# Optimization experiments

Hardware: AMD Instinct MI355X
Metric: run time of the kernel (lower is better)

Reference implementation:

```python
import jax, jax.numpy as jnp
import numpy as np

N_VOCAB, N_REL, D_EMB, D_HID, N_MOTIF = 200000, 50, 128, 128, 85
N_NODES, N_EDGES, N_CENTER, N_NONMOL = 100000, 600000, 512, 20000


def _l2norm(x):
    # torch F.normalize(p=2, dim=1) with eps=1e-12
    n = jnp.linalg.norm(x, axis=1, keepdims=True)
    return x / jnp.maximum(n, 1e-12)


def _gine(x, src, dst, edge_attr, W, b):
    # GINEConv(eps=0): Linear(x + segment_sum(relu(x[src] + edge_attr), dst))
    m = jax.nn.relu(x[src] + edge_attr)            # [E, H]
    agg = jax.ops.segment_sum(m, dst, num_segments=x.shape[0])  # [N, H]
    return (x + agg) @ W + b


def setup_inputs() -> dict:
    key = jax.random.key(0)
    ks = jax.random.split(key, 20)
    s = lambda k, shape, fan: jax.random.normal(k, shape, jnp.float32) * (1.0 / np.sqrt(fan))
    inp = {
        'node_ids': jax.random.randint(ks[0], (N_NODES,), 0, N_VOCAB),
        'rel_ids': jax.random.randint(ks[1], (N_EDGES,), 0, N_REL),
        'center_mol_idx': jax.random.randint(ks[2], (N_CENTER,), 0, N_NODES),
        'non_molecule_node_ids': jax.random.randint(ks[3], (N_NONMOL,), 0, N_NODES),
        'edge_index': jax.random.randint(ks[4], (2, N_EDGES), 0, N_NODES),
        # learned params (weights stored [in, out], i.e. torch W.T)
        'node_emb_table': jax.random.normal(ks[5], (N_VOCAB, D_EMB), jnp.float32),
        'rel_emb_table': jax.random.normal(ks[6], (N_REL, D_EMB), jnp.float32),
        'lin_W': s(ks[7], (D_EMB, D_HID), D_EMB), 'lin_b': jnp.zeros((D_HID,), jnp.float32),
        'W1': s(ks[8], (D_HID, D_HID), D_HID), 'b1': jnp.zeros((D_HID,), jnp.float32),
        'W2': s(ks[9], (D_HID, D_HID), D_HID), 'b2': jnp.zeros((D_HID,), jnp.float32),
        'edge_W': s(ks[10], (2 * D_HID, N_REL), 2 * D_HID), 'edge_b': jnp.zeros((N_REL,), jnp.float32),
        'motif_W': s(ks[11], (D_HID, N_MOTIF), D_HID), 'motif_b': jnp.zeros((N_MOTIF,), jnp.float32),
        'nodec_W': s(ks[12], (D_HID, 15), D_HID), 'nodec_b': jnp.zeros((15,), jnp.float32),
        'bin_W': s(ks[13], (D_HID, 1), D_HID), 'bin_b': jnp.zeros((1,), jnp.float32),
    }
    return inp


def reference(node_ids, rel_ids, center_mol_idx, non_molecule_node_ids, edge_index,
              node_emb_table, rel_emb_table, lin_W, lin_b, W1, b1, W2, b2,
              edge_W, edge_b, motif_W, motif_b, nodec_W, nodec_b, bin_W, bin_b):
    x = _l2norm(node_emb_table[node_ids])          # [N, D]
    e = _l2norm(rel_emb_table[rel_ids])            # [E, D]
    x = jax.nn.relu(x @ lin_W + lin_b)             # [N, H]
    e = jax.nn.relu(e @ lin_W + lin_b)             # [E, H]
    src, dst = edge_index[0], edge_index[1]
    x = jax.nn.relu(_gine(x, src, dst, e, W1, b1))
    x = _gine(x, src, dst, e, W2, b2)              # [N, H]
    edge_pred_input = jnp.concatenate([x[src], x[dst]], axis=1)   # [E, 2H]
    edge_class = edge_pred_input @ edge_W + edge_b                 # [E, num_rels]
    motif_pred = x[center_mol_idx] @ motif_W + motif_b             # [B, num_motifs]
    node_class = x[non_molecule_node_ids] @ nodec_W + nodec_b      # [M, 15]
    binary_pred = x @ bin_W + bin_b                                # [N, 1]
    return (edge_class, motif_pred, node_class, binary_pred)
```

## Files before the change

### kernel.cpp

```cpp
#include <hip/hip_runtime.h>
#include <hip/hip_bf16.h>
#include <math.h>

typedef __hip_bfloat16 bf16;
typedef __attribute__((ext_vector_type(8))) short short8;
typedef __attribute__((ext_vector_type(4))) float float4v;
typedef __attribute__((ext_vector_type(2))) float float2v;
typedef __attribute__((ext_vector_type(2))) unsigned short ushort2v;
typedef __attribute__((ext_vector_type(4))) unsigned short ushort4v;

#define N_NODES_C 100000
#define N_EDGES_C 600000
#define N_CENTER_C 512
#define N_NONMOL_C 20000
#define N_REL_C 50
#define D_C 128
#define N_MOTIF_C 85

#define EO_EDGE  0L
#define EO_MOTIF 30000000L
#define EO_NODEC 30043520L
#define EO_BIN   30343520L

#define AGG_OFF  0L
#define ET_OFF   51200000L
#define WT0_OFF  51225600L
#define WT1_OFF  51258368L
#define WT2_OFF  51291136L
#define BPQ_OFF  51323904L
#define LB_OFF   51352576L
#define B1_OFF   51353088L
#define B2_OFF   51353600L
#define OFFS_OFF 51354112L
#define BSUM_OFF 51755680L
#define SSRC_OFF 51757248L
#define SREL_OFF 54157248L
#define SDST_OFF 56557248L

#define EPW_C 32

__device__ __forceinline__ float b2f(bf16 v) { return __bfloat162float(v); }
__device__ __forceinline__ float bits2f(unsigned short s) {
    unsigned u = ((unsigned)s) << 16; float f; __builtin_memcpy(&f, &u, 4); return f;
}
__device__ __forceinline__ unsigned short f2bits(float f) {
    bf16 h = __float2bfloat16(f); unsigned short s; __builtin_memcpy(&s, &h, 2); return s;
}
__device__ __forceinline__ float ldf(const void* p, size_t i, int isbf) {
    return isbf ? __bfloat162float(((const bf16*)p)[i]) : ((const float*)p)[i];
}
__device__ __forceinline__ void stout_nt(void* p, size_t i, int isbf, float v) {
    if (isbf) __builtin_nontemporal_store(f2bits(v), (unsigned short*)p + i);
    else      __builtin_nontemporal_store(v, (float*)p + i);
}

__global__ void probe_kernel(const void* __restrict__ table, int* __restrict__ flag) {
    __shared__ int bad[256];
    int t = threadIdx.x;
    const bf16* p = (const bf16*)table;
    int cnt = 0;
    for (int i = 0; i < 64; i++) {
        float v = __bfloat162float(p[t * 64 + i]);
        if (!isfinite(v) || fabsf(v) > 1000.0f) cnt++;
    }
    bad[t] = cnt;
    __syncthreads();
    for (int s = 128; s > 0; s >>= 1) {
        if (t < s) bad[t] += bad[t + s];
        __syncthreads();
    }
    if (t == 0) *flag = (bad[0] == 0) ? 1 : 0;
}

__global__ void prepack_kernel(const int* __restrict__ flag,
                               const void* __restrict__ linW, const void* __restrict__ w1,
                               const void* __restrict__ w2, const void* __restrict__ edgeW,
                               const void* __restrict__ linb, const void* __restrict__ bb1,
                               const void* __restrict__ bb2,
                               unsigned short* __restrict__ WT0, unsigned short* __restrict__ WT1,
                               unsigned short* __restrict__ WT2, unsigned short* __restrict__ BPQ,
                               float* __restrict__ LB, float* __restrict__ B1p, float* __restrict__ B2p) {
    int isbf = *flag;
    int g = blockIdx.x * 256 + threadIdx.x;
    if (g < 3 * 16384) {
        int w = g / 16384, i = g % 16384;
        int n = i >> 7, k = i & 127;
        const void* src = (w == 0) ? linW : (w == 1) ? w1 : w2;
        unsigned short* dst = (w == 0) ? WT0 : (w == 1) ? WT1 : WT2;
        dst[i] = f2bits(ldf(src, (size_t)k * 128 + n, isbf));
    } else if (g < 3 * 16384 + 112 * 128) {
        int i = g - 3 * 16384;
        int j = i >> 7, k = i & 127;
        float v = 0.0f;
        if (j < 50)       v = ldf(edgeW, (size_t)k * 50 + j, isbf);
        else if (j < 100) v = ldf(edgeW, (size_t)(128 + k) * 50 + (j - 50), isbf);
        BPQ[i] = f2bits(v);
    } else if (g < 3 * 16384 + 112 * 128 + 3 * 128) {
        int i = g - (3 * 16384 + 112 * 128);
        int w = i >> 7, n = i & 127;
        const void* src = (w == 0) ? linb : (w == 1) ? bb1 : bb2;
        float* dst = (w == 0) ? LB : (w == 1) ? B1p : B2p;
        dst[n] = ldf(src, n, isbf);
    }
}

__global__ void et_kernel(const int* __restrict__ flag,
                          const void* __restrict__ table,
                          const void* __restrict__ W,
                          const void* __restrict__ bias,
                          float* __restrict__ out) {
    int isbf = *flag;
    int row = blockIdx.x;
    int t = threadIdx.x;
    float v = ldf(table, (size_t)row * D_C + t, isbf);
    __shared__ float sv[D_C];
    __shared__ float red[D_C];
    red[t] = v * v;
    __syncthreads();
    for (int s = 64; s > 0; s >>= 1) {
        if (t < s) red[t] += red[t + s];
        __syncthreads();
    }
    float nrm = fmaxf(sqrtf(red[0]), 1e-12f);
    sv[t] = v / nrm;
    __syncthreads();
    float acc = ldf(bias, t, isbf);
    for (int k = 0; k < D_C; k++) acc = fmaf(sv[k], ldf(W, k * D_C + t, isbf), acc);
    out[(size_t)row * D_C + t] = fmaxf(acc, 0.0f);
}

__global__ void normalize_kernel(const int* __restrict__ flag,
                                 const int* __restrict__ ids,
                                 const void* __restrict__ table,
                                 unsigned short* __restrict__ out) {
    int w = (int)((blockIdx.x * (long)blockDim.x + threadIdx.x) >> 6);
    int lane = threadIdx.x & 63;
    if (w >= N_NODES_C) return;
    int isbf = *flag;
    int id = ids[w];
    float v0, v1;
    if (isbf) {
        const unsigned short* p = (const unsigned short*)table + (size_t)id * D_C + lane * 2;
        ushort2 u = *(const ushort2*)p;
        v0 = bits2f(u.x); v1 = bits2f(u.y);
    } else {
        const float* p = (const float*)table + (size_t)id * D_C + lane * 2;
        float2 f = *(const float2*)p;
        v0 = f.x; v1 = f.y;
    }
    float ss = v0 * v0 + v1 * v1;
#pragma unroll
    for (int o = 32; o > 0; o >>= 1) ss += __shfl_down(ss, o, 64);
    ss = __shfl(ss, 0, 64);
    float inv = 1.0f / fmaxf(sqrtf(ss), 1e-12f);
    ushort2 o2;
    o2.x = f2bits(v0 * inv);
    o2.y = f2bits(v1 * inv);
    *(ushort2*)(out + (size_t)w * D_C + lane * 2) = o2;
}

template <int NOUT, bool RELU, bool ADD_AGG, bool HAS_BIAS>
__global__ __launch_bounds__(256, 2) void gemm_kernel(
        const unsigned short* __restrict__ X,
        const float* __restrict__ AGG,
        const unsigned short* __restrict__ BT,
        const float* __restrict__ bias,
        unsigned short* __restrict__ Y,
        int M) {
    constexpr int NT = (NOUT + 15) / 16;
    __shared__ short Als[128 * 128];
    __shared__ short Bls[NT * 16 * 128];
    int t = threadIdx.x;
    int m0 = blockIdx.x * 128;

#pragma unroll
    for (int p = 0; p < 8; p++) {
        int lin = (p * 256 + t) * 8;
        int row = lin >> 7, col = lin & 127;
        int gr = m0 + row; if (gr >= M) gr = M - 1;
        short8 xv = *(const short8*)(X + (size_t)gr * 128 + col);
        if (ADD_AGG) {
            const float* ap = AGG + (size_t)gr * 128 + col;
            float4v a0 = *(const float4v*)ap;
            float4v a1 = *(const float4v*)(ap + 4);
            short8 r;
#pragma unroll
            for (int i = 0; i < 4; i++) r[i] = (short)f2bits(bits2f((unsigned short)xv[i]) + a0[i]);
#pragma unroll
            for (int i = 0; i < 4; i++) r[4 + i] = (short)f2bits(bits2f((unsigned short)xv[4 + i]) + a1[i]);
            xv = r;
        }
        *(short8*)&Als[lin] = xv;
    }
    constexpr int BELEMS = NT * 16 * 128;
#pragma unroll
    for (int p = 0; p * 2048 < BELEMS; p++) {
        int lin = (p * 256 + t) * 8;
        if (lin < BELEMS) *(short8*)&Bls[lin] = *(const short8*)(BT + lin);
    }
    __syncthreads();

    int wave = t >> 6, lane = t & 63;
    int quad = lane >> 4, lr = lane & 15;
    int wr0 = wave * 32;

    short8 afr[2][4];
#pragma unroll
    for (int mt = 0; mt < 2; mt++)
#pragma unroll
        for (int kk = 0; kk < 4; kk++)
            afr[mt][kk] = *(short8*)&Als[(wr0 + mt * 16 + lr) * 128 + kk * 32 + quad * 8];

#pragma unroll
    for (int nt = 0; nt < NT; nt++) {
        short8 bfr[4];
#pragma unroll
        for (int kk = 0; kk < 4; kk++)
            bfr[kk] = *(short8*)&Bls[(nt * 16 + lr) * 128 + kk * 32 + quad * 8];
        int col = nt * 16 + lr;
        float bs = 0.0f;
        if (HAS_BIAS) bs = bias[col];
#pragma unroll
        for (int mt = 0; mt < 2; mt++) {
            float4v acc = {0.0f, 0.0f, 0.0f, 0.0f};
#pragma unroll
            for (int kk = 0; kk < 4; kk++)
                acc = __builtin_amdgcn_mfma_f32_16x16x32_bf16(afr[mt][kk], bfr[kk], acc, 0, 0, 0);
            int rbase = m0 + wr0 + mt * 16 + quad * 4;
#pragma unroll
            for (int r = 0; r < 4; r++) {
                int row = rbase + r;
                float v = acc[r] + bs;
                if (RELU) v = fmaxf(v, 0.0f);
                if (row < M && ((NOUT & 15) == 0 || col < NOUT))
                    Y[(size_t)row * NOUT + col] = f2bits(v);
            }
        }
    }
}

__global__ void hist_kernel(const int* __restrict__ ei, int* __restrict__ cnt) {
    int e = blockIdx.x * 256 + threadIdx.x;
    if (e < N_EDGES_C) atomicAdd(&cnt[ei[N_EDGES_C + e]], 1);
}

__global__ void scan1_kernel(int* __restrict__ cnt, int* __restrict__ bsum) {
    __shared__ int s[256];
    int t = threadIdx.x;
    int idx = blockIdx.x * 256 + t;
    int v = (idx < N_NODES_C) ? cnt[idx] : 0;
    s[t] = v;
    __syncthreads();
    for (int o = 1; o < 256; o <<= 1) {
        int u = (t >= o) ? s[t - o] : 0;
        __syncthreads();
        s[t] += u;
        __syncthreads();
    }
    if (idx < N_NODES_C) cnt[idx] = s[t] - v;
    if (t == 255) bsum[blockIdx.x] = s[255];
}

__global__ void scan2_kernel(int* __restrict__ bsum, int nb) {
    __shared__ int s[512];
    int t = threadIdx.x;
    int v = (t < nb) ? bsum[t] : 0;
    s[t] = v;
    __syncthreads();
    for (int o = 1; o < 512; o <<= 1) {
        int u = (t >= o) ? s[t - o] : 0;
        __syncthreads();
        s[t] += u;
        __syncthreads();
    }
    if (t < nb) bsum[t] = s[t] - v;
}

__global__ void scan3_kernel(int* __restrict__ cnt, const int* __restrict__ bsum) {
    int idx = blockIdx.x * 256 + threadIdx.x;
    if (idx < N_NODES_C) cnt[idx] += bsum[blockIdx.x];
}

__global__ void sort_scatter_kernel(const int* __restrict__ ei, const int* __restrict__ rel,
                                    int* __restrict__ offs,
                                    int* __restrict__ ssrc, int* __restrict__ srel,
                                    int* __restrict__ sdst) {
    int e = blockIdx.x * 256 + threadIdx.x;
    if (e >= N_EDGES_C) return;
    int dst = ei[N_EDGES_C + e];
    int pos = atomicAdd(&offs[dst], 1);
    ssrc[pos] = ei[e];
    srel[pos] = rel[e];
    sdst[pos] = dst;
}

__global__ __launch_bounds__(256) void gather_agg2_kernel(
        const unsigned short* __restrict__ x,
        const int* __restrict__ ssrc, const int* __restrict__ srel,
        const int* __restrict__ sdst,
        const float* __restrict__ etab,
        float* __restrict__ agg) {
    int w = (int)((blockIdx.x * 256u + threadIdx.x) >> 6);
    int lane = threadIdx.x & 63;
    int e0 = w * EPW_C;
    if (e0 >= N_EDGES_C) return;

    float a0 = 0.0f, a1 = 0.0f;
    int cur = sdst[e0];
    bool first = true;

    for (int e = e0; e < e0 + EPW_C; e += 8) {
        int4 sva = *(const int4*)(ssrc + e);
        int4 svb = *(const int4*)(ssrc + e + 4);
        int4 rva = *(const int4*)(srel + e);
        int4 rvb = *(const int4*)(srel + e + 4);
        int4 dva = *(const int4*)(sdst + e);
        int4 dvb = *(const int4*)(sdst + e + 4);
        int s_[8] = {sva.x, sva.y, sva.z, sva.w, svb.x, svb.y, svb.z, svb.w};
        int r_[8] = {rva.x, rva.y, rva.z, rva.w, rvb.x, rvb.y, rvb.z, rvb.w};
        int d_[8] = {dva.x, dva.y, dva.z, dva.w, dvb.x, dvb.y, dvb.z, dvb.w};
        ushort2 uu[8];
        float2 tt[8];
#pragma unroll
        for (int j = 0; j < 8; j++) uu[j] = *(const ushort2*)(x + (size_t)s_[j] * D_C + lane * 2);
#pragma unroll
        for (int j = 0; j < 8; j++) tt[j] = *(const float2*)(etab + r_[j] * D_C + lane * 2);
#pragma unroll
        for (int j = 0; j < 8; j++) {
            if (d_[j] != cur) {
                float* p = agg + (size_t)cur * D_C + lane * 2;
                if (first) { atomicAdd(p, a0); atomicAdd(p + 1, a1); }
                else       { p[0] = a0; p[1] = a1; }
                first = false; a0 = 0.0f; a1 = 0.0f; cur = d_[j];
            }
            a0 += fmaxf(bits2f(uu[j].x) + tt[j].x, 0.0f);
            a1 += fmaxf(bits2f(uu[j].y) + tt[j].y, 0.0f);
        }
    }
    bool endshere = (e0 + EPW_C >= N_EDGES_C) || (sdst[e0 + EPW_C] != cur);
    float* p = agg + (size_t)cur * D_C + lane * 2;
    if (!first && endshere) { p[0] = a0; p[1] = a1; }
    else { atomicAdd(p, a0); atomicAdd(p + 1, a1); }
}

__global__ void edge_out_kernel(const int* __restrict__ flag,
                                const int* __restrict__ ei,
                                const unsigned short* __restrict__ PQ,
                                const void* __restrict__ eb,
                                void* __restrict__ out) {
    int isbf = *flag;
    long g = (long)blockIdx.x * blockDim.x + threadIdx.x;
    if (g >= (long)N_EDGES_C * 13) return;
    int e = (int)(g / 13);
    int jq = (int)(g - (long)e * 13);
    int src = ei[e];
    int dst = ei[N_EDGES_C + e];
    if (jq < 12) {
        int j = jq * 4;
        ushort4v us = *(const ushort4v*)(PQ + (size_t)src * 100 + j);
        ushort2v ud0 = *(const ushort2v*)(PQ + (size_t)dst * 100 + 50 + j);
        ushort2v ud1 = *(const ushort2v*)(PQ + (size_t)dst * 100 + 50 + j + 2);
        float v0 = bits2f(us.x) + bits2f(ud0.x) + ldf(eb, j, isbf);
        float v1 = bits2f(us.y) + bits2f(ud0.y) + ldf(eb, j + 1, isbf);
        float v2 = bits2f(us.z) + bits2f(ud1.x) + ldf(eb, j + 2, isbf);
        float v3 = bits2f(us.w) + bits2f(ud1.y) + ldf(eb, j + 3, isbf);
        if (isbf) {
            ushort2v o0; o0.x = f2bits(v0); o0.y = f2bits(v1);
            ushort2v o1; o1.x = f2bits(v2); o1.y = f2bits(v3);
            unsigned short* ob = (unsigned short*)out + EO_EDGE + (size_t)e * 50 + j;
            __builtin_nontemporal_store(o0, (ushort2v*)ob);
            __builtin_nontemporal_store(o1, (ushort2v*)(ob + 2));
        } else {
            float2v o0; o0.x = v0; o0.y = v1;
            float2v o1; o1.x = v2; o1.y = v3;
            float* ob = (float*)out + EO_EDGE + (size_t)e * 50 + j;
            __builtin_nontemporal_store(o0, (float2v*)ob);
            __builtin_nontemporal_store(o1, (float2v*)(ob + 2));
        }
    } else {
        int j = 48;
        ushort2v us = *(const ushort2v*)(PQ + (size_t)src * 100 + j);
        ushort2v ud = *(const ushort2v*)(PQ + (size_t)dst * 100 + 50 + j);
        float v0 = bits2f(us.x) + bits2f(ud.x) + ldf(eb, j, isbf);
        float v1 = bits2f(us.y) + bits2f(ud.y) + ldf(eb, j + 1, isbf);
        if (isbf) {
            ushort2v o; o.x = f2bits(v0); o.y = f2bits(v1);
            __builtin_nontemporal_store(o, (ushort2v*)((unsigned short*)out + EO_EDGE + (size_t)e * 50 + j));
        } else {
            float2v o; o.x = v0; o.y = v1;
            __builtin_nontemporal_store(o, (float2v*)((float*)out + EO_EDGE + (size_t)e * 50 + j));
        }
    }
}

__global__ void motif_kernel(const int* __restrict__ flag,
                             const int* __restrict__ cidx,
                             const bf16* __restrict__ x,
                             const void* __restrict__ W,
                             const void* __restrict__ bias,
                             void* __restrict__ out) {
    int isbf = *flag;
    int row = blockIdx.x;
    int t = threadIdx.x;
    __shared__ float sv[D_C];
    int id = cidx[row];
    sv[t] = b2f(x[(size_t)id * D_C + t]);
    __syncthreads();
    if (t < N_MOTIF_C) {
        float acc = ldf(bias, t, isbf);
        for (int k = 0; k < D_C; k++) acc = fmaf(sv[k], ldf(W, k * N_MOTIF_C + t, isbf), acc);
        stout_nt(out, EO_MOTIF + (size_t)row * N_MOTIF_C + t, isbf, acc);
    }
}

__global__ void nodec_kernel(const int* __restrict__ flag,
                             const int* __restrict__ nidx,
                             const bf16* __restrict__ x,
                             const void* __restrict__ W,
                             const void* __restrict__ bias,
                             void* __restrict__ out) {
    int isbf = *flag;
    int g = blockIdx.x * blockDim.x + threadIdx.x;
    if (g >= N_NONMOL_C * 15) return;
    int row = g / 15;
    int j = g - row * 15;
    int id = nidx[row];
    float acc = ldf(bias, j, isbf);
    for (int k = 0; k < D_C; k++) acc = fmaf(b2f(x[(size_t)id * D_C + k]), ldf(W, k * 15 + j, isbf), acc);
    stout_nt(out, EO_NODEC + g, isbf, acc);
}

__global__ void binary_kernel(const int* __restrict__ flag,
                              const bf16* __restrict__ x,
                              const void* __restrict__ W,
                              const void* __restrict__ bias,
                              void* __restrict__ out) {
    int isbf = *flag;
    int g = blockIdx.x * blockDim.x + threadIdx.x;
    int row = g >> 6;
    int lane = threadIdx.x & 63;
    if (row >= N_NODES_C) return;
    float a = b2f(x[(size_t)row * D_C + lane]) * ldf(W, lane, isbf) +
              b2f(x[(size_t)row * D_C + 64 + lane]) * ldf(W, 64 + lane, isbf);
#pragma unroll
    for (int off = 32; off > 0; off >>= 1) a += __shfl_down(a, off, 64);
    if (lane == 0) stout_nt(out, EO_BIN + row, isbf, a + ldf(bias, 0, isbf));
}

extern "C" void kernel_launch(void* const* d_in, const int* in_sizes, int n_in,
                              void* d_out, int out_size, void* d_ws, size_t ws_size,
                              hipStream_t stream) {
    const int* node_ids = (const int*)d_in[0];
    const int* rel_ids  = (const int*)d_in[1];
    const int* center   = (const int*)d_in[2];
    const int* nonmol   = (const int*)d_in[3];
    const int* ei       = (const int*)d_in[4];
    const void* node_emb = d_in[5];
    const void* rel_emb  = d_in[6];
    const void* lin_W = d_in[7];
    const void* lin_b = d_in[8];
    const void* W1 = d_in[9];
    const void* b1 = d_in[10];
    const void* W2 = d_in[11];
    const void* b2 = d_in[12];
    const void* edge_W = d_in[13];
    const void* edge_b = d_in[14];
    const void* motif_W = d_in[15];
    const void* motif_b = d_in[16];
    const void* nodec_W = d_in[17];
    const void* nodec_b = d_in[18];
    const void* bin_W = d_in[19];
    const void* bin_b = d_in[20];

    char* wsb = (char*)d_ws;
    unsigned short* X0 = (unsigned short*)wsb;
    unsigned short* X1 = (unsigned short*)(wsb + (size_t)N_NODES_C * D_C * 2);
    int* FLAG = (int*)(wsb + (size_t)2 * N_NODES_C * D_C * 2);
    unsigned short* PQ = X1;

    char* ob = (char*)d_out;
    float* AGG = (float*)(ob + AGG_OFF);
    float* ET  = (float*)(ob + ET_OFF);
    unsigned short* WT0 = (unsigned short*)(ob + WT0_OFF);
    unsigned short* WT1 = (unsigned short*)(ob + WT1_OFF);
    unsigned short* WT2 = (unsigned short*)(ob + WT2_OFF);
    unsigned short* BPQ = (unsigned short*)(ob + BPQ_OFF);
    float* LB  = (float*)(ob + LB_OFF);
    float* B1p = (float*)(ob + B1_OFF);
    float* B2p = (float*)(ob + B2_OFF);
    int* OFFS = (int*)(ob + OFFS_OFF);
    int* BSUM = (int*)(ob + BSUM_OFF);
    int* SSRC = (int*)(ob + SSRC_OFF);
    int* SREL = (int*)(ob + SREL_OFF);
    int* SDST = (int*)(ob + SDST_OFF);

    const int gemm_blocks = (N_NODES_C + 127) / 128;
    const int nscan = (N_NODES_C + 255) / 256;
    const int eblocks = (N_EDGES_C + 255) / 256;
    const int g2_waves = N_EDGES_C / EPW_C;
    const int g2_blocks = (g2_waves + 3) / 4;

    probe_kernel<<<1, 256, 0, stream>>>(node_emb, FLAG);
    prepack_kernel<<<250, 256, 0, stream>>>(FLAG, lin_W, W1, W2, edge_W, lin_b, b1, b2,
                                            WT0, WT1, WT2, BPQ, LB, B1p, B2p);
    et_kernel<<<N_REL_C, D_C, 0, stream>>>(FLAG, rel_emb, lin_W, lin_b, ET);

    hipMemsetAsync(OFFS, 0, N_NODES_C * sizeof(int), stream);
    hist_kernel<<<eblocks, 256, 0, stream>>>(ei, OFFS);
    scan1_kernel<<<nscan, 256, 0, stream>>>(OFFS, BSUM);
    scan2_kernel<<<1, 512, 0, stream>>>(BSUM, nscan);
    scan3_kernel<<<nscan, 256, 0, stream>>>(OFFS, BSUM);
    sort_scatter_kernel<<<eblocks, 256, 0, stream>>>(ei, rel_ids, OFFS, SSRC, SREL, SDST);

    normalize_kernel<<<(N_NODES_C * 64 + 255) / 256, 256, 0, stream>>>(FLAG, node_ids, node_emb, X0);
    gemm_kernel<128, true, false, true><<<gemm_blocks, 256, 0, stream>>>(X0, nullptr, WT0, LB, X0, N_NODES_C);

    hipMemsetAsync(AGG, 0, (size_t)N_NODES_C * D_C * sizeof(float), stream);
    gather_agg2_kernel<<<g2_blocks, 256, 0, stream>>>(X0, SSRC, SREL, SDST, ET, AGG);
    gemm_kernel<128, true, true, true><<<gemm_blocks, 256, 0, stream>>>(X0, AGG, WT1, B1p, X1, N_NODES_C);

    hipMemsetAsync(AGG, 0, (size_t)N_NODES_C * D_C * sizeof(float), stream);
    gather_agg2_kernel<<<g2_blocks, 256, 0, stream>>>(X1, SSRC, SREL, SDST, ET, AGG);
    gemm_kernel<128, false, true, true><<<gemm_blocks, 256, 0, stream>>>(X1, AGG, WT2, B2p, X0, N_NODES_C);

    gemm_kernel<100, false, false, false><<<gemm_blocks, 256, 0, stream>>>(X0, nullptr, BPQ, nullptr, PQ, N_NODES_C);

    long ethreads = (long)N_EDGES_C * 13;
    edge_out_kernel<<<(int)((ethreads + 255) / 256), 256, 0, stream>>>(FLAG, ei, PQ, edge_b, d_out);

    motif_kernel<<<N_CENTER_C, D_C, 0, stream>>>(FLAG, center, (const bf16*)X0, motif_W, motif_b, d_out);
    nodec_kernel<<<(N_NONMOL_C * 15 + 255) / 256, 256, 0, stream>>>(FLAG, nonmol, (const bf16*)X0, nodec_W, nodec_b, d_out);
    binary_kernel<<<(N_NODES_C * 64 + 255) / 256, 256, 0, stream>>>(FLAG, (const bf16*)X0, bin_W, bin_b, d_out);
}
```

Measured before the change: 697.1 us.

## Partition edge waves by node boundaries and write x+agg in bf16 directly

Adds a binary-search partition kernel that assigns each wave a whole range of destination nodes, so the aggregation no longer needs float atomics or a zeroed fp32 buffer. The gather kernel now adds the residual x itself and writes bf16 x+agg, so the GEMM reads one bf16 input instead of x plus an fp32 aggregate. Both memsets are removed. In exchange, per-wave work becomes uneven, since node-aligned ranges vary in edge count. Rounding the sum to bf16 before the GEMM also adds precision loss.

```diff
diff --git a/kernel.cpp b/kernel.cpp
--- a/kernel.cpp
+++ b/kernel.cpp
@@ -22,7 +22,7 @@
 #define EO_NODEC 30043520L
 #define EO_BIN   30343520L
 
-#define AGG_OFF  0L
+#define XA_OFF   0L
 #define ET_OFF   51200000L
 #define WT0_OFF  51225600L
 #define WT1_OFF  51258368L
@@ -36,8 +36,10 @@
 #define SSRC_OFF 51757248L
 #define SREL_OFF 54157248L
 #define SDST_OFF 56557248L
+#define NLO_OFF  58957248L
 
 #define EPW_C 32
+#define NW_C (N_EDGES_C / EPW_C)
 
 __device__ __forceinline__ float b2f(bf16 v) { return __bfloat162float(v); }
 __device__ __forceinline__ float bits2f(unsigned short s) {
@@ -294,53 +296,85 @@
     sdst[pos] = dst;
 }
 
-__global__ __launch_bounds__(256) void gather_agg2_kernel(
+__global__ void wave_part_kernel(const int* __restrict__ offs, int* __restrict__ nlo) {
+    int w = blockIdx.x * 256 + threadIdx.x;
+    if (w > NW_C) return;
+    if (w == NW_C) { nlo[w] = N_NODES_C; return; }
+    int target = w * EPW_C;
+    int lo = 0, hi = N_NODES_C;
+    while (lo < hi) {
+        int mid = (lo + hi) >> 1;
+        int s = (mid == 0) ? 0 : offs[mid - 1];
+        if (s >= target) hi = mid; else lo = mid + 1;
+    }
+    nlo[w] = lo;
+}
+
+__global__ __launch_bounds__(256) void gather_fuse_kernel(
         const unsigned short* __restrict__ x,
+        const int* __restrict__ offs,
         const int* __restrict__ ssrc, const int* __restrict__ srel,
         const int* __restrict__ sdst,
+        const int* __restrict__ nlo_arr,
         const float* __restrict__ etab,
-        float* __restrict__ agg) {
+        unsigned short* __restrict__ xa) {
     int w = (int)((blockIdx.x * 256u + threadIdx.x) >> 6);
     int lane = threadIdx.x & 63;
-    int e0 = w * EPW_C;
-    if (e0 >= N_EDGES_C) return;
+    if (w >= NW_C) return;
+    int nlo = nlo_arr[w];
+    int nhi = nlo_arr[w + 1];
+    if (nlo >= nhi) return;
+    int estart = (nlo == 0) ? 0 : offs[nlo - 1];
+    int eend = offs[nhi - 1];
 
     float a0 = 0.0f, a1 = 0.0f;
-    int cur = sdst[e0];
-    bool first = true;
-
-    for (int e = e0; e < e0 + EPW_C; e += 8) {
-        int4 sva = *(const int4*)(ssrc + e);
-        int4 svb = *(const int4*)(ssrc + e + 4);
-        int4 rva = *(const int4*)(srel + e);
-        int4 rvb = *(const int4*)(srel + e + 4);
-        int4 dva = *(const int4*)(sdst + e);
-        int4 dvb = *(const int4*)(sdst + e + 4);
-        int s_[8] = {sva.x, sva.y, sva.z, sva.w, svb.x, svb.y, svb.z, svb.w};
-        int r_[8] = {rva.x, rva.y, rva.z, rva.w, rvb.x, rvb.y, rvb.z, rvb.w};
-        int d_[8] = {dva.x, dva.y, dva.z, dva.w, dvb.x, dvb.y, dvb.z, dvb.w};
-        ushort2 uu[8];
-        float2 tt[8];
-#pragma unroll
-        for (int j = 0; j < 8; j++) uu[j] = *(const ushort2*)(x + (size_t)s_[j] * D_C + lane * 2);
-#pragma unroll
-        for (int j = 0; j < 8; j++) tt[j] = *(const float2*)(etab + r_[j] * D_C + lane * 2);
-#pragma unroll
-        for (int j = 0; j < 8; j++) {
-            if (d_[j] != cur) {
-                float* p = agg + (size_t)cur * D_C + lane * 2;
-                if (first) { atomicAdd(p, a0); atomicAdd(p + 1, a1); }
-                else       { p[0] = a0; p[1] = a1; }
-                first = false; a0 = 0.0f; a1 = 0.0f; cur = d_[j];
+    int cur = (estart < eend) ? sdst[estart] : -1;
+
+    for (int e = estart; e < eend; e += 4) {
+        int s_[4], r_[4], d_[4];
+        ushort2 uu[4];
+        float2 tt[4];
+#pragma unroll
+        for (int j = 0; j < 4; j++) {
+            int idx = (e + j < eend) ? (e + j) : (eend - 1);
+            s_[j] = ssrc[idx]; r_[j] = srel[idx]; d_[j] = sdst[idx];
+        }
+#pragma unroll
+        for (int j = 0; j < 4; j++) uu[j] = *(const ushort2*)(x + (size_t)s_[j] * D_C + lane * 2);
+#pragma unroll
+        for (int j = 0; j < 4; j++) tt[j] = *(const float2*)(etab + (size_t)r_[j] * D_C + lane * 2);
+#pragma unroll
+        for (int j = 0; j < 4; j++) {
+            if (e + j < eend) {
+                if (d_[j] != cur) {
+                    ushort2 xr = *(const ushort2*)(x + (size_t)cur * D_C + lane * 2);
+                    ushort2 o;
+                    o.x = f2bits(bits2f(xr.x) + a0);
+                    o.y = f2bits(bits2f(xr.y) + a1);
+                    *(ushort2*)(xa + (size_t)cur * D_C + lane * 2) = o;
+                    a0 = 0.0f; a1 = 0.0f; cur = d_[j];
+                }
+                a0 += fmaxf(bits2f(uu[j].x) + tt[j].x, 0.0f);
+                a1 += fmaxf(bits2f(uu[j].y) + tt[j].y, 0.0f);
             }
-            a0 += fmaxf(bits2f(uu[j].x) + tt[j].x, 0.0f);
-            a1 += fmaxf(bits2f(uu[j].y) + tt[j].y, 0.0f);
-        }
-    }
-    bool endshere = (e0 + EPW_C >= N_EDGES_C) || (sdst[e0 + EPW_C] != cur);
-    float* p = agg + (size_t)cur * D_C + lane * 2;
-    if (!first && endshere) { p[0] = a0; p[1] = a1; }
-    else { atomicAdd(p, a0); atomicAdd(p + 1, a1); }
+        }
+    }
+    if (cur >= 0) {
+        ushort2 xr = *(const ushort2*)(x + (size_t)cur * D_C + lane * 2);
+        ushort2 o;
+        o.x = f2bits(bits2f(xr.x) + a0);
+        o.y = f2bits(bits2f(xr.y) + a1);
+        *(ushort2*)(xa + (size_t)cur * D_C + lane * 2) = o;
+    }
+    int prev = estart;
+    for (int nn = nlo; nn < nhi; nn++) {
+        int se = offs[nn];
+        if (se == prev) {
+            *(ushort2*)(xa + (size_t)nn * D_C + lane * 2) =
+                *(const ushort2*)(x + (size_t)nn * D_C + lane * 2);
+        }
+        prev = se;
+    }
 }
 
 __global__ void edge_out_kernel(const int* __restrict__ flag,
@@ -479,7 +513,7 @@
     unsigned short* PQ = X1;
 
     char* ob = (char*)d_out;
-    float* AGG = (float*)(ob + AGG_OFF);
+    unsigned short* XA = (unsigned short*)(ob + XA_OFF);
     float* ET  = (float*)(ob + ET_OFF);
     unsigned short* WT0 = (unsigned short*)(ob + WT0_OFF);
     unsigned short* WT1 = (unsigned short*)(ob + WT1_OFF);
@@ -493,12 +527,12 @@
     int* SSRC = (int*)(ob + SSRC_OFF);
     int* SREL = (int*)(ob + SREL_OFF);
     int* SDST = (int*)(ob + SDST_OFF);
+    int* NLO  = (int*)(ob + NLO_OFF);
 
     const int gemm_blocks = (N_NODES_C + 127) / 128;
     const int nscan = (N_NODES_C + 255) / 256;
     const int eblocks = (N_EDGES_C + 255) / 256;
-    const int g2_waves = N_EDGES_C / EPW_C;
-    const int g2_blocks = (g2_waves + 3) / 4;
+    const int g2_blocks = (NW_C + 3) / 4;
 
     probe_kernel<<<1, 256, 0, stream>>>(node_emb, FLAG);
     prepack_kernel<<<250, 256, 0, stream>>>(FLAG, lin_W, W1, W2, edge_W, lin_b, b1, b2,
@@ -511,17 +545,16 @@
     scan2_kernel<<<1, 512, 0, stream>>>(BSUM, nscan);
     scan3_kernel<<<nscan, 256, 0, stream>>>(OFFS, BSUM);
     sort_scatter_kernel<<<eblocks, 256, 0, stream>>>(ei, rel_ids, OFFS, SSRC, SREL, SDST);
+    wave_part_kernel<<<(NW_C + 1 + 255) / 256, 256, 0, stream>>>(OFFS, NLO);
 
     normalize_kernel<<<(N_NODES_C * 64 + 255) / 256, 256, 0, stream>>>(FLAG, node_ids, node_emb, X0);
     gemm_kernel<128, true, false, true><<<gemm_blocks, 256, 0, stream>>>(X0, nullptr, WT0, LB, X0, N_NODES_C);
 
-    hipMemsetAsync(AGG, 0, (size_t)N_NODES_C * D_C * sizeof(float), stream);
-    gather_agg2_kernel<<<g2_blocks, 256, 0, stream>>>(X0, SSRC, SREL, SDST, ET, AGG);
-    gemm_kernel<128, true, true, true><<<gemm_blocks, 256, 0, stream>>>(X0, AGG, WT1, B1p, X1, N_NODES_C);
-
-    hipMemsetAsync(AGG, 0, (size_t)N_NODES_C * D_C * sizeof(float), stream);
-    gather_agg2_kernel<<<g2_blocks, 256, 0, stream>>>(X1, SSRC, SREL, SDST, ET, AGG);
-    gemm_kernel<128, false, true, true><<<gemm_blocks, 256, 0, stream>>>(X1, AGG, WT2, B2p, X0, N_NODES_C);
+    gather_fuse_kernel<<<g2_blocks, 256, 0, stream>>>(X0, OFFS, SSRC, SREL, SDST, NLO, ET, XA);
+    gemm_kernel<128, true, false, true><<<gemm_blocks, 256, 0, stream>>>(XA, nullptr, WT1, B1p, X1, N_NODES_C);
+
+    gather_fuse_kernel<<<g2_blocks, 256, 0, stream>>>(X1, OFFS, SSRC, SREL, SDST, NLO, ET, XA);
+    gemm_kernel<128, false, false, true><<<gemm_blocks, 256, 0, stream>>>(XA, nullptr, WT2, B2p, X0, N_NODES_C);
 
     gemm_kernel<100, false, false, false><<<gemm_blocks, 256, 0, stream>>>(X0, nullptr, BPQ, nullptr, PQ, N_NODES_C);
 
```

Result: no change. 686.1 us (-1.6%).
